# Performance work log

Measured on AMD Instinct MI355X. Metric: run time of the kernel, lower is better.

## Reference

```python
import jax, jax.numpy as jnp
import numpy as np

PAD = 0  # padding_idx


def setup_inputs() -> dict:
    key = jax.random.key(0)
    ks = jax.random.split(key, 10)
    T, B, V, E, H = 64, 32, 32000, 512, 512
    s = 0.05
    tokens = jax.random.randint(ks[0], (T, B), 0, V).astype(jnp.int32)
    emb = jax.random.normal(ks[1], (V, E), jnp.float32) * s
    emb = emb.at[PAD].set(0.0)  # padding_idx row zeroed like nn.Embedding
    return {
        "tokens": tokens,
        "emb": emb,
        "W_ih": jax.random.normal(ks[2], (4 * H, E), jnp.float32) * s,
        "W_hh": jax.random.normal(ks[3], (4 * H, H), jnp.float32) * s,
        "b_ih": jax.random.normal(ks[4], (4 * H,), jnp.float32) * s,
        "b_hh": jax.random.normal(ks[5], (4 * H,), jnp.float32) * s,
        "W_fc": jax.random.normal(ks[6], (V, H), jnp.float32) * s,
        "b_fc": jax.random.normal(ks[7], (V,), jnp.float32) * s,
        "h0": jax.random.normal(ks[8], (B, H), jnp.float32) * s,
        "c0": jax.random.normal(ks[9], (B, H), jnp.float32) * s,
    }


def reference(tokens, emb, W_ih, W_hh, b_ih, b_hh, W_fc, b_fc, h0, c0):
    H = h0.shape[1]

    def step(carry, tok):
        h, c = carry                      # [B,H] each
        x = emb[tok]                      # [B,E] per-token embedding lookup
        gates = x @ W_ih.T + h @ W_hh.T + b_ih + b_hh  # [B,4H]
        i, f, g, o = jnp.split(gates, 4, axis=-1)
        i = jax.nn.sigmoid(i)
        f = jax.nn.sigmoid(f)
        g = jnp.tanh(g)
        o = jax.nn.sigmoid(o)
        c_tmp = f * c + i * g             # LSTMCell cell update
        h_tmp = o * jnp.tanh(c_tmp)
        mask = (tok != PAD)[:, None]      # masked state update: carry state only for non-pad tokens
        h_new = jnp.where(mask, h_tmp, h)
        c_new = jnp.where(mask, c_tmp, c)
        logits = h_tmp @ W_fc.T + b_fc    # [B,V] projection of the tentative hidden (as in source)
        return (h_new, c_new), logits

    (_, _), out = jax.lax.scan(step, (h0, c0), tokens)  # out: [T,B,V]
    return out
```

## Files before the change

### kernel.cpp

```cpp
#include <hip/hip_runtime.h>
#include <stdint.h>

#define TT 64
#define BB 32
#define VV 32000
#define EE 512
#define HH 512
#define G4 2048
#define NBLK 64

typedef float f32x4 __attribute__((ext_vector_type(4)));
typedef short bf16x8 __attribute__((ext_vector_type(8)));

__device__ __forceinline__ unsigned int f2bf(float f) {
    union { float f; uint32_t u; } v; v.f = f;
    uint32_t r = v.u + 0x7fffu + ((v.u >> 16) & 1u);
    return (r >> 16);
}
__device__ __forceinline__ uint2 pack4(float4 v) {
    uint2 o;
    o.x = f2bf(v.x) | (f2bf(v.y) << 16);
    o.y = f2bf(v.z) | (f2bf(v.w) << 16);
    return o;
}

__device__ __forceinline__ void gload16(const unsigned short* g, unsigned short* l) {
    __builtin_amdgcn_global_load_lds(
        (const __attribute__((address_space(1))) unsigned int*)g,
        (__attribute__((address_space(3))) unsigned int*)l, 16, 0, 0);
}

__global__ __launch_bounds__(256)
void prep_kernel(const float* __restrict__ emb, const int* __restrict__ tokens,
                 const float* __restrict__ h0, const float* __restrict__ Wih,
                 const float* __restrict__ Wfc,
                 unsigned short* __restrict__ Xbf, unsigned short* __restrict__ hb0,
                 unsigned short* __restrict__ Wib, unsigned short* __restrict__ Wfb,
                 unsigned int* __restrict__ syncp) {
    const int NX = TT * BB * EE / 4;
    const int NH = BB * HH / 4;
    const int NWI = G4 * EE / 4;
    const int NWF = VV * HH / 4;
    const int NS = NBLK * 16 + 16;
    const long total = (long)NX + NH + NWI + NWF + NS;
    for (long idx = (long)blockIdx.x * 256 + threadIdx.x; idx < total;
         idx += (long)gridDim.x * 256) {
        long i = idx;
        if (i < NX) {
            int rrow = (int)(i >> 7);
            int e4 = (int)(i & 127);
            int tok = tokens[rrow];
            float4 v = ((const float4*)(emb + (size_t)tok * EE))[e4];
            *(uint2*)(Xbf + (size_t)rrow * EE + e4 * 4) = pack4(v);
            continue;
        }
        i -= NX;
        if (i < NH) {
            float4 v = ((const float4*)h0)[i];
            *(uint2*)(hb0 + i * 4) = pack4(v);
            continue;
        }
        i -= NH;
        if (i < NWI) {
            float4 v = ((const float4*)Wih)[i];
            *(uint2*)(Wib + i * 4) = pack4(v);
            continue;
        }
        i -= NWI;
        if (i < NWF) {
            float4 v = ((const float4*)Wfc)[i];
            *(uint2*)(Wfb + i * 4) = pack4(v);
            continue;
        }
        i -= NWF;
        syncp[i] = 0u;
    }
}

__global__ __launch_bounds__(256, 2)
void gemm_bb(const unsigned short* __restrict__ A, const unsigned short* __restrict__ B,
             float* __restrict__ Cout, const float* __restrict__ bias1,
             const float* __restrict__ bias2, int N, int K, int ntn, int mode) {
    __shared__ unsigned short lA[128 * 64];
    __shared__ unsigned short lB[128 * 64];
    const int tid = threadIdx.x;
    const int lane = tid & 63;
    const int w = tid >> 6;
    const int nwg = gridDim.x;
    const int cpx = nwg >> 3;
    const int wid = (blockIdx.x & 7) * cpx + (blockIdx.x >> 3);
    const int m0 = (wid / ntn) * 128;
    const int n0 = (wid % ntn) * 128;
    const int wm = (w & 1) * 64;
    const int wn = (w >> 1) * 64;
    f32x4 acc[4][4];
#pragma unroll
    for (int i = 0; i < 4; ++i)
#pragma unroll
        for (int j = 0; j < 4; ++j) acc[i][j] = (f32x4){0.f, 0.f, 0.f, 0.f};

    for (int k0 = 0; k0 < K; k0 += 64) {
#pragma unroll
        for (int i = 0; i < 4; ++i) {
            int c = i * 256 + tid;
            int row = c >> 3;
            int kg = c & 7;
            gload16(A + (size_t)(m0 + row) * K + k0 + kg * 8, &lA[c * 8]);
            gload16(B + (size_t)(n0 + row) * K + k0 + kg * 8, &lB[c * 8]);
        }
        __syncthreads();
#pragma unroll
        for (int ks = 0; ks < 2; ++ks) {
            const int kgrp = ks * 4 + (lane >> 4);
            bf16x8 af[4], bfr[4];
#pragma unroll
            for (int mi = 0; mi < 4; ++mi) {
                int row = wm + mi * 16 + (lane & 15);
                af[mi] = *(const bf16x8*)&lA[row * 64 + kgrp * 8];
            }
#pragma unroll
            for (int ni = 0; ni < 4; ++ni) {
                int row = wn + ni * 16 + (lane & 15);
                bfr[ni] = *(const bf16x8*)&lB[row * 64 + kgrp * 8];
            }
#pragma unroll
            for (int mi = 0; mi < 4; ++mi)
#pragma unroll
                for (int ni = 0; ni < 4; ++ni)
                    acc[mi][ni] = __builtin_amdgcn_mfma_f32_16x16x32_bf16(
                        af[mi], bfr[ni], acc[mi][ni], 0, 0, 0);
        }
        __syncthreads();
    }
    const int col_l = lane & 15;
    const int row_l = (lane >> 4) * 4;
#pragma unroll
    for (int ni = 0; ni < 4; ++ni) {
        int col = n0 + wn + ni * 16 + col_l;
        float bv = bias1[col];
        if (bias2) bv += bias2[col];
#pragma unroll
        for (int mi = 0; mi < 4; ++mi) {
            int rowb = m0 + wm + mi * 16 + row_l;
#pragma unroll
            for (int rr = 0; rr < 4; ++rr) {
                size_t idx;
                if (mode) {
                    idx = (size_t)(rowb + rr) * N + ((col & 511) << 2) + (col >> 9);
                } else {
                    idx = (size_t)(rowb + rr) * N + col;
                }
                Cout[idx] = acc[mi][ni][rr] + bv;
            }
        }
    }
}

__global__ __launch_bounds__(256, 1)
void rec_kernel(const float* __restrict__ XG4, const float* __restrict__ Whh,
                const int* __restrict__ tokens, const float* __restrict__ h0,
                const float* __restrict__ c0, unsigned short* __restrict__ hb0,
                unsigned short* __restrict__ hb1, unsigned short* __restrict__ Htmp,
                unsigned int* __restrict__ syncp) {
    __shared__ int ltok[TT * BB];
    const int tid = threadIdx.x;
    const int l = tid & 63;
    const int w = tid >> 6;
    const int mi = w >> 1;
    const int ni = w & 1;
    const int blk = blockIdx.x;
    unsigned int* flags = syncp;
    unsigned int* go = syncp + NBLK * 16;

    for (int u = tid; u < TT * BB; u += 256) ltok[u] = tokens[u];

    const int b  = ni * 16 + (l & 15);
    const int hc = mi * 4 + (l >> 4);
    const int jh = blk * 8 + hc;

    const int r = mi * 16 + (l & 15);
    const int hcr = r >> 2;
    const int gr = r & 3;
    const int ksub = (l >> 4) * 8;
    const float* wrow = Whh + ((size_t)gr * HH + (size_t)blk * 8 + hcr) * HH;
    bf16x8 af[16];
#pragma unroll
    for (int kc = 0; kc < 16; ++kc) {
        float4 w0 = *(const float4*)(wrow + kc * 32 + ksub);
        float4 w1 = *(const float4*)(wrow + kc * 32 + ksub + 4);
        union { unsigned short s[8]; bf16x8 v; } u;
        u.s[0] = (unsigned short)f2bf(w0.x);
        u.s[1] = (unsigned short)f2bf(w0.y);
        u.s[2] = (unsigned short)f2bf(w0.z);
        u.s[3] = (unsigned short)f2bf(w0.w);
        u.s[4] = (unsigned short)f2bf(w1.x);
        u.s[5] = (unsigned short)f2bf(w1.y);
        u.s[6] = (unsigned short)f2bf(w1.z);
        u.s[7] = (unsigned short)f2bf(w1.w);
        af[kc] = u.v;
    }

    float hprev = h0[(size_t)b * HH + jh];
    float cprev = c0[(size_t)b * HH + jh];

    const float* xgp = XG4 + (size_t)b * G4 + (size_t)jh * 4;
    float4 xv = *(const float4*)xgp;
    __syncthreads();

    for (int t = 0; t < TT; ++t) {
        const unsigned short* hin = (t & 1) ? hb1 : hb0;
        unsigned short* hout = (t & 1) ? hb0 : hb1;

        const unsigned short* hrow = hin + (size_t)b * HH + ksub;
        f32x4 acc = {0.f, 0.f, 0.f, 0.f};
#pragma unroll
        for (int kc = 0; kc < 16; ++kc) {
            bf16x8 bfv = *(const bf16x8*)(hrow + kc * 32);
            acc = __builtin_amdgcn_mfma_f32_16x16x32_bf16(af[kc], bfv, acc, 0, 0, 0);
        }

        float gi = acc[0] + xv.x;
        float gf = acc[1] + xv.y;
        float gg = acc[2] + xv.z;
        float go_ = acc[3] + xv.w;
        float ig = 1.f / (1.f + __expf(-gi));
        float fg = 1.f / (1.f + __expf(-gf));
        float gt = tanhf(gg);
        float og = 1.f / (1.f + __expf(-go_));
        float c_tmp = fg * cprev + ig * gt;
        float h_tmp = og * tanhf(c_tmp);
        const bool msk = ltok[t * BB + b] != 0;
        cprev = msk ? c_tmp : cprev;
        hprev = msk ? h_tmp : hprev;

        Htmp[((size_t)t * BB + b) * HH + jh] = (unsigned short)f2bf(h_tmp);
        hout[(size_t)b * HH + jh] = (unsigned short)f2bf(hprev);

        if (t < TT - 1) {
            float4 xn = *(const float4*)(xgp + (size_t)(t + 1) * BB * G4);
            __syncthreads();
            if (blk == 0) {
                if (tid > 0 && tid < NBLK) {
                    while (__hip_atomic_load(&flags[tid * 16], __ATOMIC_RELAXED,
                                             __HIP_MEMORY_SCOPE_AGENT) <= (unsigned)t)
                        __builtin_amdgcn_s_sleep(1);
                }
                __syncthreads();
                if (tid == 0) {
                    __builtin_amdgcn_fence(__ATOMIC_ACQUIRE, "agent");
                    __hip_atomic_store(go, (unsigned)(t + 1), __ATOMIC_RELEASE,
                                       __HIP_MEMORY_SCOPE_AGENT);
                }
            } else {
                if (tid == 0) {
                    __hip_atomic_store(&flags[blk * 16], (unsigned)(t + 1),
                                       __ATOMIC_RELEASE, __HIP_MEMORY_SCOPE_AGENT);
                    while (__hip_atomic_load(go, __ATOMIC_RELAXED,
                                             __HIP_MEMORY_SCOPE_AGENT) <= (unsigned)t)
                        __builtin_amdgcn_s_sleep(1);
                    __builtin_amdgcn_fence(__ATOMIC_ACQUIRE, "agent");
                }
            }
            __syncthreads();
            xv = xn;
        }
    }
}

extern "C" void kernel_launch(void* const* d_in, const int* in_sizes, int n_in,
                              void* d_out, int out_size, void* d_ws, size_t ws_size,
                              hipStream_t stream) {
    const int*   tokens = (const int*)d_in[0];
    const float* emb    = (const float*)d_in[1];
    const float* W_ih   = (const float*)d_in[2];
    const float* W_hh   = (const float*)d_in[3];
    const float* b_ih   = (const float*)d_in[4];
    const float* b_hh   = (const float*)d_in[5];
    const float* W_fc   = (const float*)d_in[6];
    const float* b_fc   = (const float*)d_in[7];
    const float* h0     = (const float*)d_in[8];
    const float* c0     = (const float*)d_in[9];

    char* ws = (char*)d_ws;
    size_t o = 0;
    unsigned short* Xbf  = (unsigned short*)(ws + o); o += (size_t)TT * BB * EE * 2;
    unsigned short* Htmp = (unsigned short*)(ws + o); o += (size_t)TT * BB * HH * 2;
    float* XG = (float*)(ws + o); o += (size_t)TT * BB * G4 * 4;
    unsigned short* Wib = (unsigned short*)(ws + o); o += (size_t)G4 * EE * 2;
    unsigned short* Wfb = (unsigned short*)(ws + o); o += (size_t)VV * HH * 2;
    unsigned short* hb0 = (unsigned short*)(ws + o); o += (size_t)BB * HH * 2;
    unsigned short* hb1 = (unsigned short*)(ws + o); o += (size_t)BB * HH * 2;
    unsigned int* syncp = (unsigned int*)(ws + o); o += (NBLK * 16 + 16) * 4;
    (void)ws_size; (void)in_sizes; (void)n_in; (void)out_size;

    prep_kernel<<<2048, 256, 0, stream>>>(emb, tokens, h0, W_ih, W_fc,
                                          Xbf, hb0, Wib, Wfb, syncp);
    gemm_bb<<<(G4 / 128) * ((TT * BB) / 128), 256, 0, stream>>>(
        Xbf, Wib, XG, b_ih, b_hh, G4, EE, G4 / 128, 1);
    rec_kernel<<<NBLK, 256, 0, stream>>>(XG, W_hh, tokens, h0, c0, hb0, hb1,
                                         Htmp, syncp);
    gemm_bb<<<(VV / 128) * ((TT * BB) / 128), 256, 0, stream>>>(
        Htmp, Wfb, (float*)d_out, b_fc, nullptr, VV, HH, VV / 128, 0);
}
```

Before: 875.5 us.

## Replace centralized grid barrier with all-to-all flags and atomic h exchange

```diff
diff --git a/kernel.cpp b/kernel.cpp
--- a/kernel.cpp
+++ b/kernel.cpp
@@ -80,7 +80,7 @@
 __global__ __launch_bounds__(256, 2)
 void gemm_bb(const unsigned short* __restrict__ A, const unsigned short* __restrict__ B,
              float* __restrict__ Cout, const float* __restrict__ bias1,
-             const float* __restrict__ bias2, int N, int K, int ntn, int mode) {
+             const float* __restrict__ bias2, int N, int K, int ntm, int mode) {
     __shared__ unsigned short lA[128 * 64];
     __shared__ unsigned short lB[128 * 64];
     const int tid = threadIdx.x;
@@ -89,8 +89,8 @@
     const int nwg = gridDim.x;
     const int cpx = nwg >> 3;
     const int wid = (blockIdx.x & 7) * cpx + (blockIdx.x >> 3);
-    const int m0 = (wid / ntn) * 128;
-    const int n0 = (wid % ntn) * 128;
+    const int m0 = (wid % ntm) * 128;
+    const int n0 = (wid / ntm) * 128;
     const int wm = (w & 1) * 64;
     const int wn = (w >> 1) * 64;
     f32x4 acc[4][4];
@@ -159,8 +159,8 @@
 __global__ __launch_bounds__(256, 1)
 void rec_kernel(const float* __restrict__ XG4, const float* __restrict__ Whh,
                 const int* __restrict__ tokens, const float* __restrict__ h0,
-                const float* __restrict__ c0, unsigned short* __restrict__ hb0,
-                unsigned short* __restrict__ hb1, unsigned short* __restrict__ Htmp,
+                const float* __restrict__ c0, unsigned int* __restrict__ hb0,
+                unsigned int* __restrict__ hb1, unsigned short* __restrict__ Htmp,
                 unsigned int* __restrict__ syncp) {
     __shared__ int ltok[TT * BB];
     const int tid = threadIdx.x;
@@ -170,7 +170,6 @@
     const int ni = w & 1;
     const int blk = blockIdx.x;
     unsigned int* flags = syncp;
-    unsigned int* go = syncp + NBLK * 16;
 
     for (int u = tid; u < TT * BB; u += 256) ltok[u] = tokens[u];
 
@@ -205,18 +204,24 @@
 
     const float* xgp = XG4 + (size_t)b * G4 + (size_t)jh * 4;
     float4 xv = *(const float4*)xgp;
+
+    const int hwbase = b * (HH / 2) + (l >> 4) * 4;
     __syncthreads();
 
     for (int t = 0; t < TT; ++t) {
-        const unsigned short* hin = (t & 1) ? hb1 : hb0;
-        unsigned short* hout = (t & 1) ? hb0 : hb1;
-
-        const unsigned short* hrow = hin + (size_t)b * HH + ksub;
+        const unsigned int* hin = (t & 1) ? hb1 : hb0;
+        unsigned int* hout = (t & 1) ? hb0 : hb1;
+
         f32x4 acc = {0.f, 0.f, 0.f, 0.f};
 #pragma unroll
         for (int kc = 0; kc < 16; ++kc) {
-            bf16x8 bfv = *(const bf16x8*)(hrow + kc * 32);
-            acc = __builtin_amdgcn_mfma_f32_16x16x32_bf16(af[kc], bfv, acc, 0, 0, 0);
+            const unsigned int* hp = hin + hwbase + kc * 16;
+            union { unsigned int u[4]; bf16x8 v; } hu;
+            hu.u[0] = __hip_atomic_load(hp + 0, __ATOMIC_RELAXED, __HIP_MEMORY_SCOPE_AGENT);
+            hu.u[1] = __hip_atomic_load(hp + 1, __ATOMIC_RELAXED, __HIP_MEMORY_SCOPE_AGENT);
+            hu.u[2] = __hip_atomic_load(hp + 2, __ATOMIC_RELAXED, __HIP_MEMORY_SCOPE_AGENT);
+            hu.u[3] = __hip_atomic_load(hp + 3, __ATOMIC_RELAXED, __HIP_MEMORY_SCOPE_AGENT);
+            acc = __builtin_amdgcn_mfma_f32_16x16x32_bf16(af[kc], hu.v, acc, 0, 0, 0);
         }
 
         float gi = acc[0] + xv.x;
@@ -234,32 +239,25 @@
         hprev = msk ? h_tmp : hprev;
 
         Htmp[((size_t)t * BB + b) * HH + jh] = (unsigned short)f2bf(h_tmp);
-        hout[(size_t)b * HH + jh] = (unsigned short)f2bf(hprev);
+
+        unsigned int h2 = f2bf(hprev);
+        unsigned int hi16 = (unsigned int)__shfl_down((int)h2, 16);
+        if (((l >> 4) & 1) == 0) {
+            __hip_atomic_store(&hout[(b * HH + jh) >> 1], h2 | (hi16 << 16),
+                               __ATOMIC_RELAXED, __HIP_MEMORY_SCOPE_AGENT);
+        }
 
         if (t < TT - 1) {
             float4 xn = *(const float4*)(xgp + (size_t)(t + 1) * BB * G4);
             __syncthreads();
-            if (blk == 0) {
-                if (tid > 0 && tid < NBLK) {
-                    while (__hip_atomic_load(&flags[tid * 16], __ATOMIC_RELAXED,
-                                             __HIP_MEMORY_SCOPE_AGENT) <= (unsigned)t)
-                        __builtin_amdgcn_s_sleep(1);
+            if (w == 0) {
+                if (l == 0) {
+                    __hip_atomic_store(&flags[blk * 16], (unsigned)(t + 1),
+                                       __ATOMIC_RELAXED, __HIP_MEMORY_SCOPE_AGENT);
                 }
-                __syncthreads();
-                if (tid == 0) {
-                    __builtin_amdgcn_fence(__ATOMIC_ACQUIRE, "agent");
-                    __hip_atomic_store(go, (unsigned)(t + 1), __ATOMIC_RELEASE,
-                                       __HIP_MEMORY_SCOPE_AGENT);
-                }
-            } else {
-                if (tid == 0) {
-                    __hip_atomic_store(&flags[blk * 16], (unsigned)(t + 1),
-                                       __ATOMIC_RELEASE, __HIP_MEMORY_SCOPE_AGENT);
-                    while (__hip_atomic_load(go, __ATOMIC_RELAXED,
-                                             __HIP_MEMORY_SCOPE_AGENT) <= (unsigned)t)
-                        __builtin_amdgcn_s_sleep(1);
-                    __builtin_amdgcn_fence(__ATOMIC_ACQUIRE, "agent");
-                }
+                while (__hip_atomic_load(&flags[l * 16], __ATOMIC_RELAXED,
+                                         __HIP_MEMORY_SCOPE_AGENT) <= (unsigned)t)
+                    __builtin_amdgcn_s_sleep(1);
             }
             __syncthreads();
             xv = xn;
@@ -296,9 +294,10 @@
     prep_kernel<<<2048, 256, 0, stream>>>(emb, tokens, h0, W_ih, W_fc,
                                           Xbf, hb0, Wib, Wfb, syncp);
     gemm_bb<<<(G4 / 128) * ((TT * BB) / 128), 256, 0, stream>>>(
-        Xbf, Wib, XG, b_ih, b_hh, G4, EE, G4 / 128, 1);
-    rec_kernel<<<NBLK, 256, 0, stream>>>(XG, W_hh, tokens, h0, c0, hb0, hb1,
+        Xbf, Wib, XG, b_ih, b_hh, G4, EE, (TT * BB) / 128, 1);
+    rec_kernel<<<NBLK, 256, 0, stream>>>(XG, W_hh, tokens, h0, c0,
+                                         (unsigned int*)hb0, (unsigned int*)hb1,
                                          Htmp, syncp);
     gemm_bb<<<(VV / 128) * ((TT * BB) / 128), 256, 0, stream>>>(
-        Htmp, Wfb, (float*)d_out, b_fc, nullptr, VV, HH, VV / 128, 0);
-}
+        Htmp, Wfb, (float*)d_out, b_fc, nullptr, VV, HH, (TT * BB) / 128, 0);
+}
```

New measurement: 1.026 ms. 17.2% more time.
